# Performance work log

Hardware: AMD Instinct MI355X
Metric: run time of the kernel (lower is better)

## Reference

```python
import jax, jax.numpy as jnp
import numpy as np

N_NODES = 50000
N_EDGES = 800000
IN_DIM = 128
HID = 64
HEADS = 4
OUT = 16
N_GRAPHS = 500
NEG_SLOPE = 0.2


def setup_inputs() -> dict:
    key = jax.random.key(0)
    ks = jax.random.split(key, 12)
    x = jax.random.normal(ks[0], (N_NODES, IN_DIM), dtype=jnp.float32)
    edge_index = jax.random.randint(ks[1], (2, N_EDGES), 0, N_NODES, dtype=jnp.int64)
    batch = jnp.sort(jax.random.randint(ks[2], (N_NODES,), 0, N_GRAPHS, dtype=jnp.int64))
    s1 = 1.0 / np.sqrt(IN_DIM)
    s2 = 1.0 / np.sqrt(HID)
    W1 = jax.random.normal(ks[3], (IN_DIM, HEADS * HID), dtype=jnp.float32) * s1
    a1_src = jax.random.normal(ks[4], (HEADS, HID), dtype=jnp.float32) * s2
    a1_dst = jax.random.normal(ks[5], (HEADS, HID), dtype=jnp.float32) * s2
    b1 = jnp.zeros((HID,), dtype=jnp.float32)
    W2 = jax.random.normal(ks[6], (HID, HEADS * HID), dtype=jnp.float32) * s2
    a2_src = jax.random.normal(ks[7], (HEADS, HID), dtype=jnp.float32) * s2
    a2_dst = jax.random.normal(ks[8], (HEADS, HID), dtype=jnp.float32) * s2
    b2 = jnp.zeros((HID,), dtype=jnp.float32)
    fcW = jax.random.normal(ks[9], (HID, OUT), dtype=jnp.float32) * s2
    fcb = jnp.zeros((OUT,), dtype=jnp.float32)
    return {"x": x, "edge_index": edge_index, "batch": batch,
            "W1": W1, "a1_src": a1_src, "a1_dst": a1_dst, "b1": b1,
            "W2": W2, "a2_src": a2_src, "a2_dst": a2_dst, "b2": b2,
            "fcW": fcW, "fcb": fcb}


def gat_conv(x, W, a_src, a_dst, b, src, dst):
    # PyG GATConv with concat=False: per-head linear, edge softmax over dst, head-mean.
    n = x.shape[0]
    h = (x @ W).reshape(n, HEADS, HID)          # [N,H,D]
    alpha_s = jnp.sum(h * a_src, axis=-1)        # [N,H]
    alpha_d = jnp.sum(h * a_dst, axis=-1)        # [N,H]
    e = jax.nn.leaky_relu(alpha_s[src] + alpha_d[dst], NEG_SLOPE)  # [E,H]
    emax = jax.ops.segment_max(e, dst, num_segments=n)
    ex = jnp.exp(e - emax[dst])
    denom = jax.ops.segment_sum(ex, dst, num_segments=n)
    alpha = ex / denom[dst]                      # [E,H], edge softmax per dst
    msg = h[src] * alpha[:, :, None]             # [E,H,D]
    out = jax.ops.segment_sum(msg, dst, num_segments=n)  # [N,H,D]
    return out.mean(axis=1) + b                  # concat=False -> head mean


def reference(x, edge_index, batch, W1, a1_src, a1_dst, b1, W2, a2_src, a2_dst, b2, fcW, fcb):
    n = x.shape[0]
    # PyG GATConv default add_self_loops=True
    loops = jnp.arange(n, dtype=edge_index.dtype)
    src = jnp.concatenate([edge_index[0], loops])
    dst = jnp.concatenate([edge_index[1], loops])
    h = jax.nn.relu(gat_conv(x, W1, a1_src, a1_dst, b1, src, dst))
    h = jax.nn.relu(gat_conv(h, W2, a2_src, a2_dst, b2, src, dst))
    # global_mean_pool over batch ids
    sums = jax.ops.segment_sum(h, batch, num_segments=N_GRAPHS)
    counts = jax.ops.segment_sum(jnp.ones((n,), dtype=h.dtype), batch, num_segments=N_GRAPHS)
    pooled = sums / jnp.clip(counts, 1.0)[:, None]
    return pooled @ fcW + fcb
```

## Files before the change

### kernel.cpp

```cpp
#include <hip/hip_runtime.h>
#include <hip/hip_bf16.h>
#include <hip/hip_fp16.h>

#define NN 50000
#define EE 800000
#define ETOT 850000
#define NG 500
#define NBLK ((NN + 255) / 256)
#define EB ((ETOT + 255) / 256)

typedef __attribute__((ext_vector_type(8))) short bf16x8;
typedef __attribute__((ext_vector_type(4))) float f32x4;
typedef _Float16 h2f __attribute__((ext_vector_type(2)));

__device__ __forceinline__ h2f as_h2(unsigned u) {
    union { unsigned u; h2f h; } x;
    x.u = u;
    return x.h;
}

__device__ __forceinline__ unsigned short bf16_rne(float v) {
    unsigned u = __float_as_uint(v);
    unsigned r = u + 0x7FFFu + ((u >> 16) & 1u);
    return (unsigned short)(r >> 16);
}

__device__ __forceinline__ int detect_stride(const int* __restrict__ ei,
                                             int tid, int* sflag) {
    if (tid < 64) {
        unsigned long long b = __ballot(ei[2 * tid + 1] != 0);
        if (tid == 0) *sflag = b ? 1 : 2;
    }
    __syncthreads();
    return *sflag;
}

__device__ __forceinline__ void prepw_one(const float* __restrict__ W,
                                          const float* __restrict__ asrc,
                                          const float* __restrict__ adst,
                                          unsigned short* __restrict__ bhi,
                                          unsigned short* __restrict__ blo,
                                          float* __restrict__ ap,
                                          float* __restrict__ adp,
                                          int K, int t) {
    int j = t / K, k = t - j * K;
    int d = j >> 2, h = j & 3;
    float v = W[k * 256 + h * 64 + d];
    unsigned short hb = bf16_rne(v);
    float hf = __uint_as_float((unsigned)hb << 16);
    bhi[t] = hb;
    blo[t] = bf16_rne(v - hf);
    if (k == 0) { ap[j] = asrc[h * 64 + d]; adp[j] = adst[h * 64 + d]; }
}

__global__ __launch_bounds__(256) void k_prep(
        const int* __restrict__ ei, int* __restrict__ src32,
        int* __restrict__ dst32, int* __restrict__ deg,
        const float* __restrict__ W1, const float* __restrict__ a1s,
        const float* __restrict__ a1d, const float* __restrict__ W2,
        const float* __restrict__ a2s, const float* __restrict__ a2d,
        unsigned short* __restrict__ b1h, unsigned short* __restrict__ b1l,
        unsigned short* __restrict__ b2h, unsigned short* __restrict__ b2l,
        float* __restrict__ ap1, float* __restrict__ adp1,
        float* __restrict__ ap2, float* __restrict__ adp2) {
    int blk = blockIdx.x;
    if (blk >= EB) {
        int g = blk - EB;
        if (g < 128)
            prepw_one(W1, a1s, a1d, b1h, b1l, ap1, adp1, 128, g * 256 + threadIdx.x);
        else
            prepw_one(W2, a2s, a2d, b2h, b2l, ap2, adp2, 64, (g - 128) * 256 + threadIdx.x);
        return;
    }
    __shared__ int sflag;
    int tid = threadIdx.x;
    int st = detect_stride(ei, tid, &sflag);
    int e = blk * 256 + tid;
    if (e >= ETOT) return;
    int s, d;
    if (e < EE) {
        s = ei[(size_t)st * e];
        d = ei[(size_t)st * (EE + e)];
    } else {
        s = d = e - EE;
    }
    src32[e] = s;
    dst32[e] = d;
    atomicAdd(&deg[d], 1);
}

__global__ __launch_bounds__(256) void k_blocksum(const int* __restrict__ deg,
                                                  int* __restrict__ bsum) {
    __shared__ int l[256];
    int gid = blockIdx.x * 256 + threadIdx.x;
    int tid = threadIdx.x;
    l[tid] = (gid < NN) ? deg[gid] : 0;
    __syncthreads();
    for (int o = 128; o > 0; o >>= 1) {
        if (tid < o) l[tid] += l[tid + o];
        __syncthreads();
    }
    if (tid == 0) bsum[blockIdx.x] = l[0];
}

__global__ __launch_bounds__(256) void k_scan_final(const int* __restrict__ deg,
                                                    const int* __restrict__ bsum,
                                                    int* __restrict__ rowptr,
                                                    int* __restrict__ cursor) {
    __shared__ int lb[256];
    __shared__ int l[256];
    int tid = threadIdx.x;
    int vb = (tid < NBLK) ? bsum[tid] : 0;
    lb[tid] = vb;
    __syncthreads();
    for (int d = 1; d < 256; d <<= 1) {
        int t = (tid >= d) ? lb[tid - d] : 0;
        __syncthreads();
        lb[tid] += t;
        __syncthreads();
    }
    int boffb = lb[blockIdx.x] - bsum[blockIdx.x];
    int gid = blockIdx.x * 256 + tid;
    int v = (gid < NN) ? deg[gid] : 0;
    l[tid] = v;
    __syncthreads();
    for (int d = 1; d < 256; d <<= 1) {
        int t = (tid >= d) ? l[tid - d] : 0;
        __syncthreads();
        l[tid] += t;
        __syncthreads();
    }
    int ex = l[tid] - v + boffb;
    if (gid < NN) { rowptr[gid] = ex; cursor[gid] = ex; }
    if (gid == 0) rowptr[NN] = ETOT;
}

__global__ __launch_bounds__(256) void k_scatter(const int* __restrict__ src32,
                                                 const int* __restrict__ dst32,
                                                 int* __restrict__ cursor,
                                                 int* __restrict__ csr_src) {
    int e = blockIdx.x * 256 + threadIdx.x;
    if (e >= ETOT) return;
    int pos = atomicAdd(&cursor[dst32[e]], 1);
    csr_src[pos] = src32[e];
}

template <int K>
__global__ __launch_bounds__(64) void k_gemm_mfma(
        const float* __restrict__ A,
        const unsigned short* __restrict__ Bhi,
        const unsigned short* __restrict__ Blo,
        const float* __restrict__ aperm,
        const float* __restrict__ adperm,
        __half* __restrict__ C16,
        float* __restrict__ os,
        float* __restrict__ od, int M) {
    const int NC = K / 32;
    int lane = threadIdx.x;
    int l = lane & 15, q = lane >> 4;
    int m0 = blockIdx.x * 32;

    bf16x8 ahi[2][NC], alo[2][NC];
#pragma unroll
    for (int t = 0; t < 2; ++t) {
        int row = m0 + t * 16 + l;
        if (row >= M) row = M - 1;
        const float* arow = A + (size_t)row * K + q * 8;
#pragma unroll
        for (int c = 0; c < NC; ++c) {
            float4 v0 = *(const float4*)(arow + c * 32);
            float4 v1 = *(const float4*)(arow + c * 32 + 4);
            float vv[8] = {v0.x, v0.y, v0.z, v0.w, v1.x, v1.y, v1.z, v1.w};
#pragma unroll
            for (int j = 0; j < 8; ++j) {
                unsigned short hb = bf16_rne(vv[j]);
                float hf = __uint_as_float((unsigned)hb << 16);
                ahi[t][c][j] = (short)hb;
                alo[t][c][j] = (short)bf16_rne(vv[j] - hf);
            }
        }
    }

    float ps[2][4] = {}, pd[2][4] = {};
    const size_t brow = (size_t)l * K + q * 8;
#pragma unroll 2
    for (int n = 0; n < 16; ++n) {
        const unsigned short* bh = Bhi + (size_t)(n * 16) * K + brow;
        const unsigned short* bl = Blo + (size_t)(n * 16) * K + brow;
        bf16x8 bhf[NC], blf[NC];
#pragma unroll
        for (int c = 0; c < NC; ++c) {
            bhf[c] = *(const bf16x8*)(bh + c * 32);
            blf[c] = *(const bf16x8*)(bl + c * 32);
        }
        f32x4 acc0 = {0.f, 0.f, 0.f, 0.f}, acc1 = {0.f, 0.f, 0.f, 0.f};
#pragma unroll
        for (int c = 0; c < NC; ++c) {
            acc0 = __builtin_amdgcn_mfma_f32_16x16x32_bf16(ahi[0][c], bhf[c], acc0, 0, 0, 0);
            acc1 = __builtin_amdgcn_mfma_f32_16x16x32_bf16(ahi[1][c], bhf[c], acc1, 0, 0, 0);
            acc0 = __builtin_amdgcn_mfma_f32_16x16x32_bf16(ahi[0][c], blf[c], acc0, 0, 0, 0);
            acc1 = __builtin_amdgcn_mfma_f32_16x16x32_bf16(ahi[1][c], blf[c], acc1, 0, 0, 0);
            acc0 = __builtin_amdgcn_mfma_f32_16x16x32_bf16(alo[0][c], bhf[c], acc0, 0, 0, 0);
            acc1 = __builtin_amdgcn_mfma_f32_16x16x32_bf16(alo[1][c], bhf[c], acc1, 0, 0, 0);
        }
        float av = aperm[n * 16 + l], dv = adperm[n * 16 + l];
#pragma unroll
        for (int r = 0; r < 4; ++r) {
            ps[0][r] += acc0[r] * av; pd[0][r] += acc0[r] * dv;
            ps[1][r] += acc1[r] * av; pd[1][r] += acc1[r] * dv;
            int gm0 = m0 + q * 4 + r;
            if (gm0 < M) C16[(size_t)gm0 * 256 + n * 16 + l] = __float2half(acc0[r]);
            int gm1 = m0 + 16 + q * 4 + r;
            if (gm1 < M) C16[(size_t)gm1 * 256 + n * 16 + l] = __float2half(acc1[r]);
        }
    }
#pragma unroll
    for (int t = 0; t < 2; ++t)
#pragma unroll
        for (int r = 0; r < 4; ++r) {
            ps[t][r] += __shfl_xor(ps[t][r], 4);
            ps[t][r] += __shfl_xor(ps[t][r], 8);
            pd[t][r] += __shfl_xor(pd[t][r], 4);
            pd[t][r] += __shfl_xor(pd[t][r], 8);
        }
    if (l < 4) {
#pragma unroll
        for (int t = 0; t < 2; ++t)
#pragma unroll
            for (int r = 0; r < 4; ++r) {
                int gm = m0 + t * 16 + q * 4 + r;
                if (gm < M) {
                    os[(size_t)gm * 4 + l] = ps[t][r];
                    od[(size_t)gm * 4 + l] = pd[t][r];
                }
            }
    }
}

__device__ __forceinline__ float lrelu_exp(float x) {
    x = x > 0.f ? x : 0.2f * x;
    return __expf(x);
}

__global__ __launch_bounds__(256) void k_aggr(const int* __restrict__ rowptr,
                                              const int* __restrict__ csr_src,
                                              const float* __restrict__ as_,
                                              const float* __restrict__ ad_,
                                              const __half* __restrict__ h16,
                                              const float* __restrict__ bias,
                                              float* __restrict__ out) {
    __shared__ uint2 als16[4][64];
    __shared__ int sss[4][64];
    int w = threadIdx.x >> 6;
    int lane = threadIdx.x & 63;
    int d = blockIdx.x * 4 + w;
    if (d >= NN) return;
    int beg = rowptr[d], end = rowptr[d + 1];
    float4 adv = *(const float4*)(ad_ + d * 4);

    int s0 = 0;
    float4 u0 = make_float4(0.f, 0.f, 0.f, 0.f);
    float4 den = make_float4(0.f, 0.f, 0.f, 0.f);
    int i0 = beg + lane;
    if (i0 < end) {
        s0 = csr_src[i0];
        float4 sv = *(const float4*)(as_ + s0 * 4);
        u0.x = lrelu_exp(sv.x + adv.x);
        u0.y = lrelu_exp(sv.y + adv.y);
        u0.z = lrelu_exp(sv.z + adv.z);
        u0.w = lrelu_exp(sv.w + adv.w);
        den = u0;
    }
    for (int i = i0 + 64; i < end; i += 64) {
        int s = csr_src[i];
        float4 sv = *(const float4*)(as_ + s * 4);
        den.x += lrelu_exp(sv.x + adv.x);
        den.y += lrelu_exp(sv.y + adv.y);
        den.z += lrelu_exp(sv.z + adv.z);
        den.w += lrelu_exp(sv.w + adv.w);
    }
#pragma unroll
    for (int off = 32; off > 0; off >>= 1) {
        den.x += __shfl_xor(den.x, off);
        den.y += __shfl_xor(den.y, off);
        den.z += __shfl_xor(den.z, off);
        den.w += __shfl_xor(den.w, off);
    }
    float4 dinv = make_float4(0.25f / den.x, 0.25f / den.y,
                              0.25f / den.z, 0.25f / den.w);
    {
        __half2 q0 = __floats2half2_rn(u0.x * dinv.x, u0.y * dinv.y);
        __half2 q1 = __floats2half2_rn(u0.z * dinv.z, u0.w * dinv.w);
        als16[w][lane] = make_uint2(*(unsigned*)&q0, *(unsigned*)&q1);
        sss[w][lane] = s0;
    }

    int cnt = end - beg;
    if (cnt > 64) cnt = 64;
    int cnt4 = (cnt + 3) & ~3;
    float acc = 0.f;
    int4 sq = *(const int4*)&sss[w][0];
    uint2 r0 = *(const uint2*)(h16 + (size_t)sq.x * 256 + lane * 4);
    uint2 r1 = *(const uint2*)(h16 + (size_t)sq.y * 256 + lane * 4);
    uint2 r2 = *(const uint2*)(h16 + (size_t)sq.z * 256 + lane * 4);
    uint2 r3 = *(const uint2*)(h16 + (size_t)sq.w * 256 + lane * 4);
    for (int j = 0; j < cnt4; j += 4) {
        int jn = (j + 4) & 63;
        int4 sn = *(const int4*)&sss[w][jn];
        uint2 n0 = *(const uint2*)(h16 + (size_t)sn.x * 256 + lane * 4);
        uint2 n1 = *(const uint2*)(h16 + (size_t)sn.y * 256 + lane * 4);
        uint2 n2 = *(const uint2*)(h16 + (size_t)sn.z * 256 + lane * 4);
        uint2 n3 = *(const uint2*)(h16 + (size_t)sn.w * 256 + lane * 4);
        uint4 A01 = *(const uint4*)&als16[w][j];
        uint4 A23 = *(const uint4*)&als16[w][j + 2];
        acc = __builtin_amdgcn_fdot2(as_h2(r0.x), as_h2(A01.x), acc, false);
        acc = __builtin_amdgcn_fdot2(as_h2(r0.y), as_h2(A01.y), acc, false);
        acc = __builtin_amdgcn_fdot2(as_h2(r1.x), as_h2(A01.z), acc, false);
        acc = __builtin_amdgcn_fdot2(as_h2(r1.y), as_h2(A01.w), acc, false);
        acc = __builtin_amdgcn_fdot2(as_h2(r2.x), as_h2(A23.x), acc, false);
        acc = __builtin_amdgcn_fdot2(as_h2(r2.y), as_h2(A23.y), acc, false);
        acc = __builtin_amdgcn_fdot2(as_h2(r3.x), as_h2(A23.z), acc, false);
        acc = __builtin_amdgcn_fdot2(as_h2(r3.y), as_h2(A23.w), acc, false);
        r0 = n0; r1 = n1; r2 = n2; r3 = n3;
    }
    for (int chunk = beg + 64; chunk < end; chunk += 64) {
        int i = chunk + lane;
        int s = 0;
        float4 al = make_float4(0.f, 0.f, 0.f, 0.f);
        if (i < end) {
            s = csr_src[i];
            float4 sv = *(const float4*)(as_ + s * 4);
            al.x = lrelu_exp(sv.x + adv.x) * dinv.x;
            al.y = lrelu_exp(sv.y + adv.y) * dinv.y;
            al.z = lrelu_exp(sv.z + adv.z) * dinv.z;
            al.w = lrelu_exp(sv.w + adv.w) * dinv.w;
        }
        int cc = end - chunk;
        if (cc > 64) cc = 64;
        for (int j = 0; j < cc; ++j) {
            int sj = __shfl(s, j);
            float a0 = __shfl(al.x, j), a1 = __shfl(al.y, j);
            float a2 = __shfl(al.z, j), a3 = __shfl(al.w, j);
            uint2 raw = *(const uint2*)(h16 + (size_t)sj * 256 + lane * 4);
            float2 fa = __half22float2(*(const __half2*)&raw.x);
            float2 fb = __half22float2(*(const __half2*)&raw.y);
            acc += a0 * fa.x + a1 * fa.y + a2 * fb.x + a3 * fb.y;
        }
    }
    float v = acc + bias[lane];
    out[d * 64 + lane] = v > 0.f ? v : 0.f;
}

__global__ __launch_bounds__(256) void k_pool_fc(const float* __restrict__ x3,
                                                 const int* __restrict__ batch,
                                                 const int* __restrict__ ei,
                                                 const float* __restrict__ fcW,
                                                 const float* __restrict__ fcb,
                                                 float* __restrict__ out) {
    __shared__ int sflag;
    int tid = threadIdx.x, lane = tid & 63, w = tid >> 6;
    int st = detect_stride(ei, tid, &sflag);
    int g = blockIdx.x;
    int lo = 0, hi = NN;
    while (lo < hi) { int mid = (lo + hi) >> 1; if (batch[(size_t)st * mid] < g) lo = mid + 1; else hi = mid; }
    int start = lo;
    hi = NN;
    while (lo < hi) { int mid = (lo + hi) >> 1; if (batch[(size_t)st * mid] < g + 1) lo = mid + 1; else hi = mid; }
    int end = lo;
    float sum = 0.f;
    for (int n = start + w; n < end; n += 4) sum += x3[n * 64 + lane];
    __shared__ float ls[4][64];
    ls[w][lane] = sum;
    __syncthreads();
    if (w == 0) {
        float c = (float)(end - start);
        if (c < 1.f) c = 1.f;
        float p = (ls[0][lane] + ls[1][lane] + ls[2][lane] + ls[3][lane]) / c;
#pragma unroll
        for (int o = 0; o < 16; ++o) {
            float v = p * fcW[lane * 16 + o];
#pragma unroll
            for (int off = 32; off > 0; off >>= 1) v += __shfl_down(v, off);
            if (lane == 0) out[g * 16 + o] = v + fcb[o];
        }
    }
}

extern "C" void kernel_launch(void* const* d_in, const int* in_sizes, int n_in,
                              void* d_out, int out_size, void* d_ws, size_t ws_size,
                              hipStream_t stream) {
    const float* x   = (const float*)d_in[0];
    const int*   ei  = (const int*)d_in[1];
    const int*   bat = (const int*)d_in[2];
    const float* W1  = (const float*)d_in[3];
    const float* a1s = (const float*)d_in[4];
    const float* a1d = (const float*)d_in[5];
    const float* b1  = (const float*)d_in[6];
    const float* W2  = (const float*)d_in[7];
    const float* a2s = (const float*)d_in[8];
    const float* a2d = (const float*)d_in[9];
    const float* b2  = (const float*)d_in[10];
    const float* fcW = (const float*)d_in[11];
    const float* fcb = (const float*)d_in[12];
    float* out = (float*)d_out;

    float* ws = (float*)d_ws;
    __half* h16  = (__half*)(ws + 256);
    float* as_   = (float*)(h16 + (size_t)NN * 256);
    float* ad_   = as_ + NN * 4;
    float* xacc  = ad_ + NN * 4;
    int* src32   = (int*)(xacc + (size_t)NN * 64);
    int* dst32   = src32 + ETOT;
    int* deg     = dst32 + ETOT;
    int* rowptr  = deg + NN;
    int* cursor  = rowptr + NN + 1;
    int* csr_src = cursor + NN;
    int* bsum    = csr_src + ETOT;
    char* p = (char*)(bsum + NBLK);
    p = (char*)(((size_t)p + 255) & ~(size_t)255);
    unsigned short* bt1h = (unsigned short*)p; p += 256 * 128 * 2;
    unsigned short* bt1l = (unsigned short*)p; p += 256 * 128 * 2;
    unsigned short* bt2h = (unsigned short*)p; p += 256 * 64 * 2;
    unsigned short* bt2l = (unsigned short*)p; p += 256 * 64 * 2;
    float* ap1  = (float*)p; p += 256 * 4;
    float* adp1 = (float*)p; p += 256 * 4;
    float* ap2  = (float*)p; p += 256 * 4;
    float* adp2 = (float*)p; p += 256 * 4;

    const int wb = (NN * 64 + 255) / 256;

    hipMemsetAsync(deg, 0, NN * sizeof(int), stream);
    k_prep<<<EB + 192, 256, 0, stream>>>(ei, src32, dst32, deg,
                                         W1, a1s, a1d, W2, a2s, a2d,
                                         bt1h, bt1l, bt2h, bt2l,
                                         ap1, adp1, ap2, adp2);
    k_blocksum<<<NBLK, 256, 0, stream>>>(deg, bsum);
    k_scan_final<<<NBLK, 256, 0, stream>>>(deg, bsum, rowptr, cursor);
    k_scatter<<<EB, 256, 0, stream>>>(src32, dst32, cursor, csr_src);

    const int gg = (NN + 31) / 32;
    k_gemm_mfma<128><<<gg, 64, 0, stream>>>(x, bt1h, bt1l, ap1, adp1, h16, as_, ad_, NN);
    k_aggr<<<wb, 256, 0, stream>>>(rowptr, csr_src, as_, ad_, h16, b1, xacc);
    k_gemm_mfma<64><<<gg, 64, 0, stream>>>(xacc, bt2h, bt2l, ap2, adp2, h16, as_, ad_, NN);
    k_aggr<<<wb, 256, 0, stream>>>(rowptr, csr_src, as_, ad_, h16, b2, xacc);
    k_pool_fc<<<NG, 256, 0, stream>>>(xacc, bat, ei, fcW, fcb, out);
}
```

Measured before the change: 380.0 us.

## Split GAT aggregation into edge-alpha kernel and column-panel aggregation kernel

Edge softmax weights are now computed once per layer by a separate kernel and stored as fp16 per edge. Aggregation is launched as 8 column panels per destination group, with each wave spreading 8 edges across lanes and reducing through shuffles. The goal is better gather locality, since each panel touches only a 32-element slice of the h rows, and more parallelism for low-degree nodes. In exchange it adds an extra launch, an alpha buffer written and read in global memory, and each panel block reloads the CSR indices and alpha.

```diff
diff --git a/kernel.cpp b/kernel.cpp
--- a/kernel.cpp
+++ b/kernel.cpp
@@ -242,29 +242,23 @@
     return __expf(x);
 }
 
-__global__ __launch_bounds__(256) void k_aggr(const int* __restrict__ rowptr,
-                                              const int* __restrict__ csr_src,
-                                              const float* __restrict__ as_,
-                                              const float* __restrict__ ad_,
-                                              const __half* __restrict__ h16,
-                                              const float* __restrict__ bias,
-                                              float* __restrict__ out) {
-    __shared__ uint2 als16[4][64];
-    __shared__ int sss[4][64];
+__global__ __launch_bounds__(256) void k_alpha(const int* __restrict__ rowptr,
+                                               const int* __restrict__ csr_src,
+                                               const float* __restrict__ as_,
+                                               const float* __restrict__ ad_,
+                                               __half* __restrict__ alpha16) {
     int w = threadIdx.x >> 6;
     int lane = threadIdx.x & 63;
     int d = blockIdx.x * 4 + w;
     if (d >= NN) return;
     int beg = rowptr[d], end = rowptr[d + 1];
     float4 adv = *(const float4*)(ad_ + d * 4);
-
-    int s0 = 0;
     float4 u0 = make_float4(0.f, 0.f, 0.f, 0.f);
     float4 den = make_float4(0.f, 0.f, 0.f, 0.f);
     int i0 = beg + lane;
     if (i0 < end) {
-        s0 = csr_src[i0];
-        float4 sv = *(const float4*)(as_ + s0 * 4);
+        int s = csr_src[i0];
+        float4 sv = *(const float4*)(as_ + s * 4);
         u0.x = lrelu_exp(sv.x + adv.x);
         u0.y = lrelu_exp(sv.y + adv.y);
         u0.z = lrelu_exp(sv.z + adv.z);
@@ -274,10 +268,15 @@
     for (int i = i0 + 64; i < end; i += 64) {
         int s = csr_src[i];
         float4 sv = *(const float4*)(as_ + s * 4);
-        den.x += lrelu_exp(sv.x + adv.x);
-        den.y += lrelu_exp(sv.y + adv.y);
-        den.z += lrelu_exp(sv.z + adv.z);
-        den.w += lrelu_exp(sv.w + adv.w);
+        float4 u;
+        u.x = lrelu_exp(sv.x + adv.x);
+        u.y = lrelu_exp(sv.y + adv.y);
+        u.z = lrelu_exp(sv.z + adv.z);
+        u.w = lrelu_exp(sv.w + adv.w);
+        __half2 q0 = __floats2half2_rn(fminf(u.x, 60000.f), fminf(u.y, 60000.f));
+        __half2 q1 = __floats2half2_rn(fminf(u.z, 60000.f), fminf(u.w, 60000.f));
+        *(uint2*)(alpha16 + (size_t)i * 4) = make_uint2(*(unsigned*)&q0, *(unsigned*)&q1);
+        den.x += u.x; den.y += u.y; den.z += u.z; den.w += u.w;
     }
 #pragma unroll
     for (int off = 32; off > 0; off >>= 1) {
@@ -288,67 +287,65 @@
     }
     float4 dinv = make_float4(0.25f / den.x, 0.25f / den.y,
                               0.25f / den.z, 0.25f / den.w);
-    {
+    if (i0 < end) {
         __half2 q0 = __floats2half2_rn(u0.x * dinv.x, u0.y * dinv.y);
         __half2 q1 = __floats2half2_rn(u0.z * dinv.z, u0.w * dinv.w);
-        als16[w][lane] = make_uint2(*(unsigned*)&q0, *(unsigned*)&q1);
-        sss[w][lane] = s0;
-    }
-
-    int cnt = end - beg;
-    if (cnt > 64) cnt = 64;
-    int cnt4 = (cnt + 3) & ~3;
+        *(uint2*)(alpha16 + (size_t)i0 * 4) = make_uint2(*(unsigned*)&q0, *(unsigned*)&q1);
+    }
+    for (int i = i0 + 64; i < end; i += 64) {
+        uint2 r = *(const uint2*)(alpha16 + (size_t)i * 4);
+        float2 fa = __half22float2(*(const __half2*)&r.x);
+        float2 fb = __half22float2(*(const __half2*)&r.y);
+        __half2 q0 = __floats2half2_rn(fa.x * dinv.x, fa.y * dinv.y);
+        __half2 q1 = __floats2half2_rn(fb.x * dinv.z, fb.y * dinv.w);
+        *(uint2*)(alpha16 + (size_t)i * 4) = make_uint2(*(unsigned*)&q0, *(unsigned*)&q1);
+    }
+}
+
+__global__ __launch_bounds__(256) void k_aggr_panel(
+        const int* __restrict__ rowptr, const int* __restrict__ csr_src,
+        const __half* __restrict__ alpha16, const __half* __restrict__ h16,
+        const float* __restrict__ bias, float* __restrict__ out) {
+    int p = blockIdx.x & 7;
+    int t = blockIdx.x >> 3;
+    int w = threadIdx.x >> 6, lane = threadIdx.x & 63;
+    int e8 = lane >> 3, dim8 = lane & 7;
+    int d = t * 4 + w;
+    if (d >= NN) return;
+    int beg = rowptr[d], end = rowptr[d + 1];
+    const __half* hsl = h16 + p * 32 + dim8 * 4;
     float acc = 0.f;
-    int4 sq = *(const int4*)&sss[w][0];
-    uint2 r0 = *(const uint2*)(h16 + (size_t)sq.x * 256 + lane * 4);
-    uint2 r1 = *(const uint2*)(h16 + (size_t)sq.y * 256 + lane * 4);
-    uint2 r2 = *(const uint2*)(h16 + (size_t)sq.z * 256 + lane * 4);
-    uint2 r3 = *(const uint2*)(h16 + (size_t)sq.w * 256 + lane * 4);
-    for (int j = 0; j < cnt4; j += 4) {
-        int jn = (j + 4) & 63;
-        int4 sn = *(const int4*)&sss[w][jn];
-        uint2 n0 = *(const uint2*)(h16 + (size_t)sn.x * 256 + lane * 4);
-        uint2 n1 = *(const uint2*)(h16 + (size_t)sn.y * 256 + lane * 4);
-        uint2 n2 = *(const uint2*)(h16 + (size_t)sn.z * 256 + lane * 4);
-        uint2 n3 = *(const uint2*)(h16 + (size_t)sn.w * 256 + lane * 4);
-        uint4 A01 = *(const uint4*)&als16[w][j];
-        uint4 A23 = *(const uint4*)&als16[w][j + 2];
-        acc = __builtin_amdgcn_fdot2(as_h2(r0.x), as_h2(A01.x), acc, false);
-        acc = __builtin_amdgcn_fdot2(as_h2(r0.y), as_h2(A01.y), acc, false);
-        acc = __builtin_amdgcn_fdot2(as_h2(r1.x), as_h2(A01.z), acc, false);
-        acc = __builtin_amdgcn_fdot2(as_h2(r1.y), as_h2(A01.w), acc, false);
-        acc = __builtin_amdgcn_fdot2(as_h2(r2.x), as_h2(A23.x), acc, false);
-        acc = __builtin_amdgcn_fdot2(as_h2(r2.y), as_h2(A23.y), acc, false);
-        acc = __builtin_amdgcn_fdot2(as_h2(r3.x), as_h2(A23.z), acc, false);
-        acc = __builtin_amdgcn_fdot2(as_h2(r3.y), as_h2(A23.w), acc, false);
-        r0 = n0; r1 = n1; r2 = n2; r3 = n3;
-    }
-    for (int chunk = beg + 64; chunk < end; chunk += 64) {
-        int i = chunk + lane;
-        int s = 0;
-        float4 al = make_float4(0.f, 0.f, 0.f, 0.f);
-        if (i < end) {
-            s = csr_src[i];
-            float4 sv = *(const float4*)(as_ + s * 4);
-            al.x = lrelu_exp(sv.x + adv.x) * dinv.x;
-            al.y = lrelu_exp(sv.y + adv.y) * dinv.y;
-            al.z = lrelu_exp(sv.z + adv.z) * dinv.z;
-            al.w = lrelu_exp(sv.w + adv.w) * dinv.w;
-        }
-        int cc = end - chunk;
-        if (cc > 64) cc = 64;
-        for (int j = 0; j < cc; ++j) {
-            int sj = __shfl(s, j);
-            float a0 = __shfl(al.x, j), a1 = __shfl(al.y, j);
-            float a2 = __shfl(al.z, j), a3 = __shfl(al.w, j);
-            uint2 raw = *(const uint2*)(h16 + (size_t)sj * 256 + lane * 4);
-            float2 fa = __half22float2(*(const __half2*)&raw.x);
-            float2 fb = __half22float2(*(const __half2*)&raw.y);
-            acc += a0 * fa.x + a1 * fa.y + a2 * fb.x + a3 * fb.y;
-        }
-    }
-    float v = acc + bias[lane];
-    out[d * 64 + lane] = v > 0.f ? v : 0.f;
+    int i = beg + e8;
+    bool ok = i < end;
+    int s = 0;
+    uint2 a2 = make_uint2(0u, 0u);
+    if (ok) {
+        s = csr_src[i];
+        a2 = *(const uint2*)(alpha16 + (size_t)i * 4);
+    }
+    while (__any(ok)) {
+        int i2 = i + 8;
+        bool ok2 = i2 < end;
+        int s2 = 0;
+        uint2 a22 = make_uint2(0u, 0u);
+        if (ok2) {
+            s2 = csr_src[i2];
+            a22 = *(const uint2*)(alpha16 + (size_t)i2 * 4);
+        }
+        if (ok) {
+            uint2 hv = *(const uint2*)(hsl + (size_t)s * 256);
+            acc = __builtin_amdgcn_fdot2(as_h2(hv.x), as_h2(a2.x), acc, false);
+            acc = __builtin_amdgcn_fdot2(as_h2(hv.y), as_h2(a2.y), acc, false);
+        }
+        i = i2; ok = ok2; s = s2; a2 = a22;
+    }
+    acc += __shfl_xor(acc, 8);
+    acc += __shfl_xor(acc, 16);
+    acc += __shfl_xor(acc, 32);
+    if (e8 == 0) {
+        float v = acc + bias[p * 8 + dim8];
+        out[(size_t)d * 64 + p * 8 + dim8] = v > 0.f ? v : 0.f;
+    }
 }
 
 __global__ __launch_bounds__(256) void k_pool_fc(const float* __restrict__ x3,
@@ -426,8 +423,10 @@
     float* adp1 = (float*)p; p += 256 * 4;
     float* ap2  = (float*)p; p += 256 * 4;
     float* adp2 = (float*)p; p += 256 * 4;
-
-    const int wb = (NN * 64 + 255) / 256;
+    p = (char*)(((size_t)p + 255) & ~(size_t)255);
+    __half* alpha16 = (__half*)p; p += (size_t)ETOT * 4 * 2;
+
+    const int wb = (NN + 3) / 4;
 
     hipMemsetAsync(deg, 0, NN * sizeof(int), stream);
     k_prep<<<EB + 192, 256, 0, stream>>>(ei, src32, dst32, deg,
@@ -440,8 +439,10 @@
 
     const int gg = (NN + 31) / 32;
     k_gemm_mfma<128><<<gg, 64, 0, stream>>>(x, bt1h, bt1l, ap1, adp1, h16, as_, ad_, NN);
-    k_aggr<<<wb, 256, 0, stream>>>(rowptr, csr_src, as_, ad_, h16, b1, xacc);
+    k_alpha<<<wb, 256, 0, stream>>>(rowptr, csr_src, as_, ad_, alpha16);
+    k_aggr_panel<<<wb * 8, 256, 0, stream>>>(rowptr, csr_src, alpha16, h16, b1, xacc);
     k_gemm_mfma<64><<<gg, 64, 0, stream>>>(xacc, bt2h, bt2l, ap2, adp2, h16, as_, ad_, NN);
-    k_aggr<<<wb, 256, 0, stream>>>(rowptr, csr_src, as_, ad_, h16, b2, xacc);
+    k_alpha<<<wb, 256, 0, stream>>>(rowptr, csr_src, as_, ad_, alpha16);
+    k_aggr_panel<<<wb * 8, 256, 0, stream>>>(rowptr, csr_src, alpha16, h16, b2, xacc);
     k_pool_fc<<<NG, 256, 0, stream>>>(xacc, bat, ei, fcW, fcb, out);
 }
```

Measured after the change: 592.6 us. 55.9% more time.

## Split degree histogram and scatter cursors into 16 per-class copies to cut atomic contention

Applied to the files above, without the earlier changes.

The degree histogram and the CSR scatter cursors are replicated into 16 copies, selected by block index, so atomics from different blocks land on separate addresses. The blocksum kernel reduces the 16 copies into the degree, and the scan kernel writes per-copy cursor offsets so the scatter stays consistent. In exchange it memsets and reads 16x larger arrays (about 3.2 MB each), and the per-copy atomics are still spread randomly across memory.

```diff
diff --git a/kernel.cpp b/kernel.cpp
--- a/kernel.cpp
+++ b/kernel.cpp
@@ -8,6 +8,7 @@
 #define NG 500
 #define NBLK ((NN + 255) / 256)
 #define EB ((ETOT + 255) / 256)
+#define NCLS 16
 
 typedef __attribute__((ext_vector_type(8))) short bf16x8;
 typedef __attribute__((ext_vector_type(4))) float f32x4;
@@ -55,7 +56,7 @@
 
 __global__ __launch_bounds__(256) void k_prep(
         const int* __restrict__ ei, int* __restrict__ src32,
-        int* __restrict__ dst32, int* __restrict__ deg,
+        int* __restrict__ dst32, int* __restrict__ degc,
         const float* __restrict__ W1, const float* __restrict__ a1s,
         const float* __restrict__ a1d, const float* __restrict__ W2,
         const float* __restrict__ a2s, const float* __restrict__ a2d,
@@ -86,15 +87,22 @@
     }
     src32[e] = s;
     dst32[e] = d;
-    atomicAdd(&deg[d], 1);
-}
-
-__global__ __launch_bounds__(256) void k_blocksum(const int* __restrict__ deg,
+    atomicAdd(&degc[(size_t)(blk & (NCLS - 1)) * NN + d], 1);
+}
+
+__global__ __launch_bounds__(256) void k_blocksum(const int* __restrict__ degc,
+                                                  int* __restrict__ deg,
                                                   int* __restrict__ bsum) {
     __shared__ int l[256];
     int gid = blockIdx.x * 256 + threadIdx.x;
     int tid = threadIdx.x;
-    l[tid] = (gid < NN) ? deg[gid] : 0;
+    int s = 0;
+    if (gid < NN) {
+#pragma unroll
+        for (int c = 0; c < NCLS; ++c) s += degc[(size_t)c * NN + gid];
+        deg[gid] = s;
+    }
+    l[tid] = s;
     __syncthreads();
     for (int o = 128; o > 0; o >>= 1) {
         if (tid < o) l[tid] += l[tid + o];
@@ -106,7 +114,8 @@
 __global__ __launch_bounds__(256) void k_scan_final(const int* __restrict__ deg,
                                                     const int* __restrict__ bsum,
                                                     int* __restrict__ rowptr,
-                                                    int* __restrict__ cursor) {
+                                                    const int* __restrict__ degc,
+                                                    int* __restrict__ cur16) {
     __shared__ int lb[256];
     __shared__ int l[256];
     int tid = threadIdx.x;
@@ -131,17 +140,26 @@
         __syncthreads();
     }
     int ex = l[tid] - v + boffb;
-    if (gid < NN) { rowptr[gid] = ex; cursor[gid] = ex; }
+    if (gid < NN) {
+        rowptr[gid] = ex;
+        int running = ex;
+#pragma unroll
+        for (int c = 0; c < NCLS; ++c) {
+            cur16[(size_t)c * NN + gid] = running;
+            running += degc[(size_t)c * NN + gid];
+        }
+    }
     if (gid == 0) rowptr[NN] = ETOT;
 }
 
 __global__ __launch_bounds__(256) void k_scatter(const int* __restrict__ src32,
                                                  const int* __restrict__ dst32,
-                                                 int* __restrict__ cursor,
+                                                 int* __restrict__ cur16,
                                                  int* __restrict__ csr_src) {
     int e = blockIdx.x * 256 + threadIdx.x;
     if (e >= ETOT) return;
-    int pos = atomicAdd(&cursor[dst32[e]], 1);
+    int c = blockIdx.x & (NCLS - 1);
+    int pos = atomicAdd(&cur16[(size_t)c * NN + dst32[e]], 1);
     csr_src[pos] = src32[e];
 }
 
@@ -413,8 +431,7 @@
     int* dst32   = src32 + ETOT;
     int* deg     = dst32 + ETOT;
     int* rowptr  = deg + NN;
-    int* cursor  = rowptr + NN + 1;
-    int* csr_src = cursor + NN;
+    int* csr_src = rowptr + NN + 1;
     int* bsum    = csr_src + ETOT;
     char* p = (char*)(bsum + NBLK);
     p = (char*)(((size_t)p + 255) & ~(size_t)255);
@@ -426,17 +443,20 @@
     float* adp1 = (float*)p; p += 256 * 4;
     float* ap2  = (float*)p; p += 256 * 4;
     float* adp2 = (float*)p; p += 256 * 4;
+    p = (char*)(((size_t)p + 255) & ~(size_t)255);
+    int* degc  = (int*)p; p += (size_t)NCLS * NN * 4;
+    int* cur16 = (int*)p; p += (size_t)NCLS * NN * 4;
 
     const int wb = (NN * 64 + 255) / 256;
 
-    hipMemsetAsync(deg, 0, NN * sizeof(int), stream);
-    k_prep<<<EB + 192, 256, 0, stream>>>(ei, src32, dst32, deg,
+    hipMemsetAsync(degc, 0, (size_t)NCLS * NN * sizeof(int), stream);
+    k_prep<<<EB + 192, 256, 0, stream>>>(ei, src32, dst32, degc,
                                          W1, a1s, a1d, W2, a2s, a2d,
                                          bt1h, bt1l, bt2h, bt2l,
                                          ap1, adp1, ap2, adp2);
-    k_blocksum<<<NBLK, 256, 0, stream>>>(deg, bsum);
-    k_scan_final<<<NBLK, 256, 0, stream>>>(deg, bsum, rowptr, cursor);
-    k_scatter<<<EB, 256, 0, stream>>>(src32, dst32, cursor, csr_src);
+    k_blocksum<<<NBLK, 256, 0, stream>>>(degc, deg, bsum);
+    k_scan_final<<<NBLK, 256, 0, stream>>>(deg, bsum, rowptr, degc, cur16);
+    k_scatter<<<EB, 256, 0, stream>>>(src32, dst32, cur16, csr_src);
 
     const int gg = (NN + 31) / 32;
     k_gemm_mfma<128><<<gg, 64, 0, stream>>>(x, bt1h, bt1l, ap1, adp1, h16, as_, ad_, NN);
```

After: 377.0 us. Within noise of the previous version (-0.8%).
